# Performance work log

Measured on AMD Instinct MI355X. Metric: run time of the kernel, lower is better.

Reference implementation:

```python
import jax, jax.numpy as jnp
import numpy as np

MAXGRAD = 2.0


def _forward(im, defgrad, affine):
    B, H, W, C = im.shape
    dt = im.dtype
    c = jnp.asarray(MAXGRAD, dt)
    # logistic growth: c / (1 + (c-1) * exp(-x)), maps defgrad into (0, c)
    dg = c / (1.0 + (c - 1.0) * jnp.exp(-defgrad))
    # integral image -> monotone sampling grid
    x_s = jnp.cumsum(dg[..., 0], axis=2)  # cumulate along width
    y_s = jnp.cumsum(dg[..., 1], axis=1)  # cumulate along height
    grid = jnp.stack([x_s, y_s], axis=-1)  # [B,H,W,2]
    # residual affine: affine + identity, applied in homogeneous coords
    ident = jnp.array([1, 0, 0, 0, 1, 0, 0, 0, 1], dtype=dt)
    A = (affine.reshape(-1, 9) + ident).reshape(B, 3, 3)
    grid3 = jnp.concatenate([grid, jnp.ones((B, H, W, 1), dt)], axis=-1)
    grid3 = jnp.einsum('bhwk,bjk->bhwj', grid3, A)  # matmul(grid, A^T)
    x = grid3[..., 0]
    y = grid3[..., 1]
    # bilinear sampling with clamped corner indices
    x0 = jnp.clip(jnp.floor(x).astype(jnp.int32), 0, W - 1)
    x1 = jnp.clip(jnp.floor(x).astype(jnp.int32) + 1, 0, W - 1)
    y0 = jnp.clip(jnp.floor(y).astype(jnp.int32), 0, H - 1)
    y1 = jnp.clip(jnp.floor(y).astype(jnp.int32) + 1, 0, H - 1)
    bidx = jnp.arange(B, dtype=jnp.int32)[:, None, None]  # batch base index
    Ia = im[bidx, y0, x0]  # [B,H,W,C]
    Ib = im[bidx, y1, x0]
    Ic = im[bidx, y0, x1]
    Id = im[bidx, y1, x1]
    x0f = x0.astype(dt); x1f = x1.astype(dt)
    y0f = y0.astype(dt); y1f = y1.astype(dt)
    wa = ((x1f - x) * (y1f - y))[..., None]
    wb = ((x1f - x) * (y - y0f))[..., None]
    wc = ((x - x0f) * (y1f - y))[..., None]
    wd = ((x - x0f) * (y - y0f))[..., None]
    out = wa * Ia + wb * Ib + wc * Ic + wd * Id
    return out, grid3


def setup_inputs() -> dict:
    key = jax.random.key(0)
    k1, k2, k3 = jax.random.split(key, 3)
    B, H, W, C = 16, 512, 512, 4
    im = jax.random.normal(k1, (B, H, W, C), dtype=jnp.float32)
    defgrad = jax.random.normal(k2, (B, H, W, 2), dtype=jnp.float32)
    affine = jax.random.normal(k3, (B, 9), dtype=jnp.float32) * 0.01
    return {"im": im, "defgrad": defgrad, "affine": affine}


def reference(im, defgrad, affine):
    return _forward(im, defgrad, affine)
```

## Files before the change

### kernel.cpp

```cpp
#include <hip/hip_runtime.h>
#include <math.h>

#define BB 16
#define HH 512
#define WW 512
#define CC 4

#define SEGS 32
#define RPT  (HH / SEGS)
#define RROWS 4

__global__ __launch_bounds__(1024)
void prep_colscan_kernel(const float2* __restrict__ defgrad,
                         float* __restrict__ dgx, int dgx_stride,
                         float* __restrict__ ys,  int ys_stride) {
    const int wt  = blockIdx.x % (WW / 32);
    const int b   = blockIdx.x / (WW / 32);
    const int col = threadIdx.x & 31;
    const int seg = threadIdx.x >> 5;
    const int w   = wt * 32 + col;
    const int h0  = seg * RPT;
    const float2* dg = defgrad + (size_t)b * HH * WW;
    const size_t rowbase = ((size_t)b * HH + h0) * WW + w;

    float vals[RPT];
    float s = 0.f;
#pragma unroll
    for (int i = 0; i < RPT; ++i) {
        float2 v = dg[(size_t)(h0 + i) * WW + w];
        float gx = 2.0f / (1.0f + expf(-v.x));
        float gy = 2.0f / (1.0f + expf(-v.y));
        dgx[(rowbase + (size_t)i * WW) * (size_t)dgx_stride] = gx;
        vals[i] = gy;
        s += gy;
    }

    __shared__ float part[SEGS][32];
    part[seg][col] = s;
    __syncthreads();

    float run = 0.f;
    for (int j = 0; j < seg; ++j) run += part[j][col];

#pragma unroll
    for (int i = 0; i < RPT; ++i) {
        run += vals[i];
        ys[(rowbase + (size_t)i * WW) * (size_t)ys_stride] = run;
    }
}

__global__ __launch_bounds__(512)
void rowscan_sample_kernel(const float4* __restrict__ im4,
                           const float*  __restrict__ dgx, int dgx_stride,
                           const float*  __restrict__ ys,  int ys_stride,
                           const float*  __restrict__ affine,
                           float4* __restrict__ out4,
                           float*  __restrict__ grid3) {
    const int blk  = blockIdx.x;
    const int gt   = (blk & 7) * ((BB * HH / RROWS) / 8) + (blk >> 3);
    const int tile = gt % (HH / RROWS);
    const int b    = gt / (HH / RROWS);

    const int w    = threadIdx.x;
    const int lane = w & 63;
    const int wv   = w >> 6;

    __shared__ float wsum[8];

    const float* Ab = affine + b * 9;
    const float a00 = Ab[0] + 1.f, a01 = Ab[1], a02 = Ab[2];
    const float a10 = Ab[3], a11 = Ab[4] + 1.f, a12 = Ab[5];
    const float a20 = Ab[6], a21 = Ab[7], a22 = Ab[8] + 1.f;

    const size_t ibase = (size_t)b * HH * WW;

    for (int r = 0; r < RROWS; ++r) {
        const int h = tile * RROWS + r;
        const size_t pix = ibase + (size_t)h * WW + w;

        float x = dgx[pix * (size_t)dgx_stride];
#pragma unroll
        for (int off = 1; off < 64; off <<= 1) {
            float n = __shfl_up(x, off, 64);
            if (lane >= off) x += n;
        }
        if (lane == 63) wsum[wv] = x;
        __syncthreads();
        float pref = 0.f;
        for (int j = 0; j < wv; ++j) pref += wsum[j];
        const float xs = x + pref;

        const float ysv = ys[pix * (size_t)ys_stride];

        const float xg = a00 * xs + a01 * ysv + a02;
        const float yg = a10 * xs + a11 * ysv + a12;
        const float wg = a20 * xs + a21 * ysv + a22;

        const int ix = (int)floorf(xg);
        const int iy = (int)floorf(yg);
        const int x0 = min(max(ix,     0), WW - 1);
        const int x1 = min(max(ix + 1, 0), WW - 1);
        const int y0 = min(max(iy,     0), HH - 1);
        const int y1 = min(max(iy + 1, 0), HH - 1);
        const float x0f = (float)x0, x1f = (float)x1;
        const float y0f = (float)y0, y1f = (float)y1;
        const float wa = (x1f - xg) * (y1f - yg);
        const float wb = (x1f - xg) * (yg - y0f);
        const float wc = (xg - x0f) * (y1f - yg);
        const float wd = (xg - x0f) * (yg - y0f);

        const float4 Ia = im4[ibase + (size_t)y0 * WW + x0];
        const float4 Ib = im4[ibase + (size_t)y1 * WW + x0];
        const float4 Ic = im4[ibase + (size_t)y0 * WW + x1];
        const float4 Id = im4[ibase + (size_t)y1 * WW + x1];

        float4 o;
        o.x = wa * Ia.x + wb * Ib.x + wc * Ic.x + wd * Id.x;
        o.y = wa * Ia.y + wb * Ib.y + wc * Ic.y + wd * Id.y;
        o.z = wa * Ia.z + wb * Ib.z + wc * Ic.z + wd * Id.z;
        o.w = wa * Ia.w + wb * Ib.w + wc * Ic.w + wd * Id.w;
        out4[pix] = o;

        grid3[pix * 3 + 0] = xg;
        grid3[pix * 3 + 1] = yg;
        grid3[pix * 3 + 2] = wg;

        __syncthreads();
    }
}

extern "C" void kernel_launch(void* const* d_in, const int* in_sizes, int n_in,
                              void* d_out, int out_size, void* d_ws, size_t ws_size,
                              hipStream_t stream) {
    const float* im      = (const float*)d_in[0];
    const float* defgrad = (const float*)d_in[1];
    const float* affine  = (const float*)d_in[2];

    float* out   = (float*)d_out;
    float* grid3 = out + (size_t)BB * HH * WW * CC;

    const size_t plane = (size_t)BB * HH * WW;
    const size_t plane_bytes = plane * sizeof(float);

    float* ys;  int ys_stride;
    float* dgx; int dgx_stride;
    if (ws_size >= 2 * plane_bytes) {
        ys  = (float*)d_ws;            ys_stride  = 1;
        dgx = (float*)d_ws + plane;    dgx_stride = 1;
    } else if (ws_size >= plane_bytes) {
        ys  = (float*)d_ws;            ys_stride  = 1;
        dgx = grid3 + 0;               dgx_stride = 3;
    } else {
        ys  = grid3 + 1;               ys_stride  = 3;
        dgx = grid3 + 0;               dgx_stride = 3;
    }

    prep_colscan_kernel<<<BB * (WW / 32), 1024, 0, stream>>>(
        (const float2*)defgrad, dgx, dgx_stride, ys, ys_stride);

    rowscan_sample_kernel<<<BB * (HH / RROWS), 512, 0, stream>>>(
        (const float4*)im, dgx, dgx_stride, ys, ys_stride, affine,
        (float4*)out, grid3);
}
```

Baseline: 261.3 us.

## Split pipeline into row-scan prep, column scan, and vectorized sampling kernels

Moves the logistic transform and the row prefix scan into a new per-row kernel, so the column-scan kernel only reads a precomputed gy plane. The sampling kernel no longer scans or synchronises; each thread handles 4 consecutive pixels with float4 loads of xs/ys and float4 stores of grid3. This removes barriers and strided 3-wide grid stores from the gather kernel. The cost is a third launch and an extra plane of intermediate traffic through the workspace.

```diff
diff --git a/kernel.cpp b/kernel.cpp
--- a/kernel.cpp
+++ b/kernel.cpp
@@ -8,32 +8,56 @@
 
 #define SEGS 32
 #define RPT  (HH / SEGS)
-#define RROWS 4
+
+__global__ __launch_bounds__(512)
+void rowprep_kernel(const float2* __restrict__ defgrad,
+                    float* __restrict__ xs, int xss,
+                    float* __restrict__ gy, int gys) {
+    const int row = blockIdx.x;
+    const int w   = threadIdx.x;
+    const size_t pix = (size_t)row * WW + w;
+
+    const float2 v = defgrad[pix];
+    const float gxv = 2.0f / (1.0f + expf(-v.x));
+    const float gyv = 2.0f / (1.0f + expf(-v.y));
+
+    const int lane = w & 63;
+    const int wv   = w >> 6;
+    float x = gxv;
+#pragma unroll
+    for (int off = 1; off < 64; off <<= 1) {
+        float n = __shfl_up(x, off, 64);
+        if (lane >= off) x += n;
+    }
+    __shared__ float wsum[8];
+    if (lane == 63) wsum[wv] = x;
+    __syncthreads();
+    float pref = 0.f;
+    for (int j = 0; j < wv; ++j) pref += wsum[j];
+
+    xs[pix * (size_t)xss] = x + pref;
+    gy[pix * (size_t)gys] = gyv;
+}
 
 __global__ __launch_bounds__(1024)
-void prep_colscan_kernel(const float2* __restrict__ defgrad,
-                         float* __restrict__ dgx, int dgx_stride,
-                         float* __restrict__ ys,  int ys_stride) {
+void colscan_kernel(const float* __restrict__ gy, int gys,
+                    float* __restrict__ ys, int yss) {
     const int wt  = blockIdx.x % (WW / 32);
     const int b   = blockIdx.x / (WW / 32);
     const int col = threadIdx.x & 31;
     const int seg = threadIdx.x >> 5;
     const int w   = wt * 32 + col;
     const int h0  = seg * RPT;
-    const float2* dg = defgrad + (size_t)b * HH * WW;
     const size_t rowbase = ((size_t)b * HH + h0) * WW + w;
 
     float vals[RPT];
+#pragma unroll
+    for (int i = 0; i < RPT; ++i)
+        vals[i] = gy[(rowbase + (size_t)i * WW) * (size_t)gys];
+
     float s = 0.f;
 #pragma unroll
-    for (int i = 0; i < RPT; ++i) {
-        float2 v = dg[(size_t)(h0 + i) * WW + w];
-        float gx = 2.0f / (1.0f + expf(-v.x));
-        float gy = 2.0f / (1.0f + expf(-v.y));
-        dgx[(rowbase + (size_t)i * WW) * (size_t)dgx_stride] = gx;
-        vals[i] = gy;
-        s += gy;
-    }
+    for (int i = 0; i < RPT; ++i) s += vals[i];
 
     __shared__ float part[SEGS][32];
     part[seg][col] = s;
@@ -45,87 +69,100 @@
 #pragma unroll
     for (int i = 0; i < RPT; ++i) {
         run += vals[i];
-        ys[(rowbase + (size_t)i * WW) * (size_t)ys_stride] = run;
-    }
-}
-
-__global__ __launch_bounds__(512)
-void rowscan_sample_kernel(const float4* __restrict__ im4,
-                           const float*  __restrict__ dgx, int dgx_stride,
-                           const float*  __restrict__ ys,  int ys_stride,
-                           const float*  __restrict__ affine,
-                           float4* __restrict__ out4,
-                           float*  __restrict__ grid3) {
-    const int blk  = blockIdx.x;
-    const int gt   = (blk & 7) * ((BB * HH / RROWS) / 8) + (blk >> 3);
-    const int tile = gt % (HH / RROWS);
-    const int b    = gt / (HH / RROWS);
-
-    const int w    = threadIdx.x;
-    const int lane = w & 63;
-    const int wv   = w >> 6;
-
-    __shared__ float wsum[8];
+        ys[(rowbase + (size_t)i * WW) * (size_t)yss] = run;
+    }
+}
+
+__global__ __launch_bounds__(1024)
+void sample_kernel(const float4* __restrict__ im4,
+                   const float*  __restrict__ xs, int xss,
+                   const float*  __restrict__ ys, int yss,
+                   const float*  __restrict__ affine,
+                   float4* __restrict__ out4,
+                   float*  __restrict__ grid3) {
+    const int blk = blockIdx.x;
+    const int gt  = (blk & 7) * 128 + (blk >> 3);
+    const int q   = gt * 1024 + threadIdx.x;
+    const size_t p0 = (size_t)q * 4;
+    const int b = (int)(p0 >> 18);
 
     const float* Ab = affine + b * 9;
     const float a00 = Ab[0] + 1.f, a01 = Ab[1], a02 = Ab[2];
     const float a10 = Ab[3], a11 = Ab[4] + 1.f, a12 = Ab[5];
     const float a20 = Ab[6], a21 = Ab[7], a22 = Ab[8] + 1.f;
 
+    float xsv[4], ysv[4];
+    if (xss == 1 && yss == 1) {
+        const float4 tx = ((const float4*)xs)[q];
+        const float4 ty = ((const float4*)ys)[q];
+        xsv[0] = tx.x; xsv[1] = tx.y; xsv[2] = tx.z; xsv[3] = tx.w;
+        ysv[0] = ty.x; ysv[1] = ty.y; ysv[2] = ty.z; ysv[3] = ty.w;
+    } else {
+#pragma unroll
+        for (int i = 0; i < 4; ++i) {
+            xsv[i] = xs[(p0 + i) * (size_t)xss];
+            ysv[i] = ys[(p0 + i) * (size_t)yss];
+        }
+    }
+
     const size_t ibase = (size_t)b * HH * WW;
-
-    for (int r = 0; r < RROWS; ++r) {
-        const int h = tile * RROWS + r;
-        const size_t pix = ibase + (size_t)h * WW + w;
-
-        float x = dgx[pix * (size_t)dgx_stride];
-#pragma unroll
-        for (int off = 1; off < 64; off <<= 1) {
-            float n = __shfl_up(x, off, 64);
-            if (lane >= off) x += n;
-        }
-        if (lane == 63) wsum[wv] = x;
-        __syncthreads();
-        float pref = 0.f;
-        for (int j = 0; j < wv; ++j) pref += wsum[j];
-        const float xs = x + pref;
-
-        const float ysv = ys[pix * (size_t)ys_stride];
-
-        const float xg = a00 * xs + a01 * ysv + a02;
-        const float yg = a10 * xs + a11 * ysv + a12;
-        const float wg = a20 * xs + a21 * ysv + a22;
-
-        const int ix = (int)floorf(xg);
-        const int iy = (int)floorf(yg);
+    float xg[4], yg[4], wgv[4], wa[4], wb[4], wc[4], wd[4];
+    size_t ia[4], ib_[4], ic[4], id[4];
+#pragma unroll
+    for (int i = 0; i < 4; ++i) {
+        xg[i]  = a00 * xsv[i] + a01 * ysv[i] + a02;
+        yg[i]  = a10 * xsv[i] + a11 * ysv[i] + a12;
+        wgv[i] = a20 * xsv[i] + a21 * ysv[i] + a22;
+        const int ix = (int)floorf(xg[i]);
+        const int iy = (int)floorf(yg[i]);
         const int x0 = min(max(ix,     0), WW - 1);
         const int x1 = min(max(ix + 1, 0), WW - 1);
         const int y0 = min(max(iy,     0), HH - 1);
         const int y1 = min(max(iy + 1, 0), HH - 1);
         const float x0f = (float)x0, x1f = (float)x1;
         const float y0f = (float)y0, y1f = (float)y1;
-        const float wa = (x1f - xg) * (y1f - yg);
-        const float wb = (x1f - xg) * (yg - y0f);
-        const float wc = (xg - x0f) * (y1f - yg);
-        const float wd = (xg - x0f) * (yg - y0f);
-
-        const float4 Ia = im4[ibase + (size_t)y0 * WW + x0];
-        const float4 Ib = im4[ibase + (size_t)y1 * WW + x0];
-        const float4 Ic = im4[ibase + (size_t)y0 * WW + x1];
-        const float4 Id = im4[ibase + (size_t)y1 * WW + x1];
-
-        float4 o;
-        o.x = wa * Ia.x + wb * Ib.x + wc * Ic.x + wd * Id.x;
-        o.y = wa * Ia.y + wb * Ib.y + wc * Ic.y + wd * Id.y;
-        o.z = wa * Ia.z + wb * Ib.z + wc * Ic.z + wd * Id.z;
-        o.w = wa * Ia.w + wb * Ib.w + wc * Ic.w + wd * Id.w;
-        out4[pix] = o;
-
-        grid3[pix * 3 + 0] = xg;
-        grid3[pix * 3 + 1] = yg;
-        grid3[pix * 3 + 2] = wg;
-
-        __syncthreads();
+        wa[i] = (x1f - xg[i]) * (y1f - yg[i]);
+        wb[i] = (x1f - xg[i]) * (yg[i] - y0f);
+        wc[i] = (xg[i] - x0f) * (y1f - yg[i]);
+        wd[i] = (xg[i] - x0f) * (yg[i] - y0f);
+        ia[i]  = ibase + (size_t)y0 * WW + x0;
+        ib_[i] = ibase + (size_t)y1 * WW + x0;
+        ic[i]  = ibase + (size_t)y0 * WW + x1;
+        id[i]  = ibase + (size_t)y1 * WW + x1;
+    }
+
+    float4 o[4];
+#pragma unroll
+    for (int i = 0; i < 4; ++i) {
+        const float4 Ia = im4[ia[i]];
+        const float4 Ib = im4[ib_[i]];
+        const float4 Ic = im4[ic[i]];
+        const float4 Id = im4[id[i]];
+        o[i].x = wa[i] * Ia.x + wb[i] * Ib.x + wc[i] * Ic.x + wd[i] * Id.x;
+        o[i].y = wa[i] * Ia.y + wb[i] * Ib.y + wc[i] * Ic.y + wd[i] * Id.y;
+        o[i].z = wa[i] * Ia.z + wb[i] * Ib.z + wc[i] * Ic.z + wd[i] * Id.z;
+        o[i].w = wa[i] * Ia.w + wb[i] * Ib.w + wc[i] * Ic.w + wd[i] * Id.w;
+    }
+
+#pragma unroll
+    for (int i = 0; i < 4; ++i) out4[p0 + i] = o[i];
+
+    if (xss == 1 && yss == 1) {
+        float4* g4 = (float4*)grid3;
+        float4 g0, g1, g2;
+        g0.x = xg[0];  g0.y = yg[0];  g0.z = wgv[0]; g0.w = xg[1];
+        g1.x = yg[1];  g1.y = wgv[1]; g1.z = xg[2];  g1.w = yg[2];
+        g2.x = wgv[2]; g2.y = xg[3];  g2.z = yg[3];  g2.w = wgv[3];
+        g4[(size_t)q * 3 + 0] = g0;
+        g4[(size_t)q * 3 + 1] = g1;
+        g4[(size_t)q * 3 + 2] = g2;
+    } else {
+#pragma unroll
+        for (int i = 0; i < 4; ++i) {
+            grid3[(p0 + i) * 3 + 0] = xg[i];
+            grid3[(p0 + i) * 3 + 1] = yg[i];
+            grid3[(p0 + i) * 3 + 2] = wgv[i];
+        }
     }
 }
 
@@ -142,23 +179,33 @@
     const size_t plane = (size_t)BB * HH * WW;
     const size_t plane_bytes = plane * sizeof(float);
 
-    float* ys;  int ys_stride;
-    float* dgx; int dgx_stride;
-    if (ws_size >= 2 * plane_bytes) {
-        ys  = (float*)d_ws;            ys_stride  = 1;
-        dgx = (float*)d_ws + plane;    dgx_stride = 1;
+    float *xsp, *ysp, *gyp;
+    int xss, yss, gys;
+    if (ws_size >= 3 * plane_bytes) {
+        xsp = (float*)d_ws;             xss = 1;
+        ysp = (float*)d_ws + plane;     yss = 1;
+        gyp = (float*)d_ws + 2 * plane; gys = 1;
+    } else if (ws_size >= 2 * plane_bytes) {
+        xsp = (float*)d_ws;             xss = 1;
+        ysp = (float*)d_ws + plane;     yss = 1;
+        gyp = grid3 + 2;                gys = 3;
     } else if (ws_size >= plane_bytes) {
-        ys  = (float*)d_ws;            ys_stride  = 1;
-        dgx = grid3 + 0;               dgx_stride = 3;
+        xsp = grid3 + 0;                xss = 3;
+        ysp = (float*)d_ws;             yss = 1;
+        gyp = grid3 + 2;                gys = 3;
     } else {
-        ys  = grid3 + 1;               ys_stride  = 3;
-        dgx = grid3 + 0;               dgx_stride = 3;
-    }
-
-    prep_colscan_kernel<<<BB * (WW / 32), 1024, 0, stream>>>(
-        (const float2*)defgrad, dgx, dgx_stride, ys, ys_stride);
-
-    rowscan_sample_kernel<<<BB * (HH / RROWS), 512, 0, stream>>>(
-        (const float4*)im, dgx, dgx_stride, ys, ys_stride, affine,
+        xsp = grid3 + 0;                xss = 3;
+        ysp = grid3 + 1;                yss = 3;
+        gyp = grid3 + 2;                gys = 3;
+    }
+
+    rowprep_kernel<<<BB * HH, 512, 0, stream>>>(
+        (const float2*)defgrad, xsp, xss, gyp, gys);
+
+    colscan_kernel<<<BB * (WW / 32), 1024, 0, stream>>>(
+        gyp, gys, ysp, yss);
+
+    sample_kernel<<<1024, 1024, 0, stream>>>(
+        (const float4*)im, xsp, xss, ysp, yss, affine,
         (float4*)out, grid3);
 }
```

After: 299.8 us. 14.7% more time.
